# Kernel optimization log

Hardware: AMD Instinct MI355X
Metric: run time of the kernel (lower is better)

Reference implementation:

```python
import jax, jax.numpy as jnp
import numpy as np

N_NODES = 50000
N_EDGES = 400000
N_GRAPHS = 512
IN_DIM = 768
HID = 64
BN_EPS = 1e-5


def setup_inputs() -> dict:
    key = jax.random.key(0)
    ks = jax.random.split(key, 12)
    x = jax.random.normal(ks[0], (N_NODES, IN_DIM), dtype=jnp.float32)
    edge_index = jax.random.randint(ks[1], (2, N_EDGES), 0, N_NODES, dtype=jnp.int64)
    batch = jnp.sort(jax.random.randint(ks[2], (N_NODES,), 0, N_GRAPHS, dtype=jnp.int64))

    def lin_init(k, fan_in, fan_out):
        kw, kb = jax.random.split(k)
        bound = 1.0 / np.sqrt(fan_in)
        W = jax.random.uniform(kw, (fan_in, fan_out), minval=-bound, maxval=bound, dtype=jnp.float32)
        b = jax.random.uniform(kb, (fan_out,), minval=-bound, maxval=bound, dtype=jnp.float32)
        return W, b

    w1a, b1a = lin_init(ks[3], IN_DIM, HID)
    w1b, b1b = lin_init(ks[4], HID, HID)
    w2a, b2a = lin_init(ks[5], HID, HID)
    w2b, b2b = lin_init(ks[6], HID, HID)
    wl, bl = lin_init(ks[7], 2 * HID, 2)

    ones = jnp.ones((HID,), jnp.float32)
    zeros = jnp.zeros((HID,), jnp.float32)
    return {
        "x": x, "edge_index": edge_index, "batch": batch,
        "w1a": w1a, "b1a": b1a, "g1": ones, "be1": zeros, "rm1": zeros, "rv1": ones,
        "w1b": w1b, "b1b": b1b,
        "w2a": w2a, "b2a": b2a, "g2": ones, "be2": zeros, "rm2": zeros, "rv2": ones,
        "w2b": w2b, "b2b": b2b,
        "wl": wl, "bl": bl,
    }


def _bn_eval(h, gamma, beta, rm, rv):
    # BatchNorm1d in eval mode: normalize with running stats
    return (h - rm) * (gamma * jax.lax.rsqrt(rv + BN_EPS)) + beta


def _gin_conv(x, src, dst, Wa, ba, gamma, beta, rm, rv, Wb, bb):
    # GINConv eps=0: h = MLP(x + sum_{j in N(i)} x_j); messages x[src] scatter-added to dst
    agg = jax.ops.segment_sum(x[src], dst, num_segments=N_NODES)
    h = x + agg
    h = jnp.dot(h, Wa) + ba
    h = jax.nn.relu(_bn_eval(h, gamma, beta, rm, rv))
    return jnp.dot(h, Wb) + bb


def reference(x, edge_index, batch,
              w1a, b1a, g1, be1, rm1, rv1, w1b, b1b,
              w2a, b2a, g2, be2, rm2, rv2, w2b, b2b,
              wl, bl):
    src, dst = edge_index[0], edge_index[1]
    # eval mode: dropout_edge and F.dropout are identity
    x1 = jax.nn.relu(_gin_conv(x, src, dst, w1a, b1a, g1, be1, rm1, rv1, w1b, b1b))
    x2 = jax.nn.relu(_gin_conv(x1, src, dst, w2a, b2a, g2, be2, rm2, rv2, w2b, b2b))
    x_jk = jnp.concatenate([x1, x2], axis=-1)  # [N, 2*HID]
    x_pool = jax.ops.segment_sum(x_jk, batch, num_segments=N_GRAPHS)  # [G, 2*HID]
    return jnp.dot(x_pool, wl) + bl  # [G, 2]
```

## Files before the change

### kernel.cpp

```cpp
#include <hip/hip_runtime.h>

constexpr int N_NODES  = 50000;
constexpr int N_EDGES  = 400000;
constexpr int N_GRAPHS = 512;
constexpr int IN_DIM   = 768;
constexpr int HID      = 64;
constexpr float BN_EPS = 1e-5f;
constexpr int CAP      = 64;

typedef __attribute__((ext_vector_type(8))) short bf16x8;
typedef __attribute__((ext_vector_type(4))) float f32x4;
typedef __attribute__((ext_vector_type(2))) float f32x2;

__device__ __forceinline__ unsigned int f2bf2(float lo, float hi) {
  unsigned int r;
  asm("v_cvt_pk_bf16_f32 %0, %1, %2" : "=v"(r) : "v"(lo), "v"(hi));
  return r;
}
__device__ __forceinline__ ushort f2bf1(float f) { return (ushort)f2bf2(f, f); }

__device__ __forceinline__ float bf2f(ushort u) {
  return __uint_as_float((unsigned int)u << 16);
}
__device__ __forceinline__ f32x2 unpk(unsigned int u) {
  f32x2 v;
  v.x = __uint_as_float(u << 16);
  v.y = __uint_as_float(u & 0xffff0000u);
  return v;
}

constexpr int W1A_E = HID * IN_DIM;
constexpr int WB_E  = HID * HID;
__global__ __launch_bounds__(256) void convert_all(
    const float* __restrict__ w1a, const float* __restrict__ w1b,
    const float* __restrict__ w2a, const float* __restrict__ w2b,
    const float* __restrict__ bl,
    ushort* __restrict__ WT, ushort* __restrict__ WT1b,
    ushort* __restrict__ WT2a, ushort* __restrict__ WT2b,
    float* __restrict__ out, int* __restrict__ cnt) {
  int i = blockIdx.x * 256 + threadIdx.x;
  if (i < W1A_E) {
    int c = i / IN_DIM, k = i - c * IN_DIM;
    WT[i] = f2bf1(w1a[(size_t)k * HID + c]);
    return;
  }
  int j = i - W1A_E;
  if (j < 3 * WB_E) {
    int w = j / WB_E, r = j - w * WB_E;
    int c = r / HID, k = r - c * HID;
    const float* W = (w == 0) ? w1b : (w == 1) ? w2a : w2b;
    ushort* D = (w == 0) ? WT1b : (w == 1) ? WT2a : WT2b;
    D[r] = f2bf1(W[(size_t)k * HID + c]);
    return;
  }
  int o = j - 3 * WB_E;
  if (o < N_GRAPHS * 2) { out[o] = bl[o & 1]; return; }
  int z = o - N_GRAPHS * 2;
  if (z < N_NODES) cnt[z] = 0;
}

constexpr int GB1 = (N_NODES + 127) / 128;
constexpr int BB  = (N_EDGES + 255) / 256;

__global__ __launch_bounds__(256) void gemm_build(const float* __restrict__ X,
                                                  const ushort* __restrict__ WT,
                                                  ushort* __restrict__ P,
                                                  const int* __restrict__ src,
                                                  const int* __restrict__ dst,
                                                  int* __restrict__ cnt,
                                                  int* __restrict__ bucket) {
  const int tid = threadIdx.x;

  if (blockIdx.x >= GB1) {
    int e = (blockIdx.x - GB1) * 256 + tid;
    if (e < N_EDGES) {
      int s = src[e];
      int d = dst[e];
      int slot = atomicAdd(&cnt[d], 1);
      if (slot < CAP) bucket[d * CAP + slot] = s << 6;
    }
    return;
  }

  __shared__ ushort xs[128][64];
  __shared__ ushort ws[64][64];
  const int row0 = blockIdx.x * 128;
  const int wave = tid >> 6, lane = tid & 63, quad = lane >> 4, l16 = lane & 15;

  const int srow = tid >> 1;
  const int sk   = (tid & 1) * 32;
  int gr = row0 + srow;
  gr = gr < N_NODES ? gr : N_NODES - 1;
  const float* xrow = &X[(size_t)gr * IN_DIM + sk];
  const int wrow = tid >> 2;
  const int wc0  = (tid & 3) * 2;
  const ushort* wrp = &WT[(size_t)wrow * IN_DIM + wc0 * 8];

  f32x4 acc[2][4] = {};

  float4 xv[8];
#pragma unroll
  for (int i = 0; i < 8; i++) xv[i] = *(const float4*)&xrow[i * 4];
  uint4 wv0 = *(const uint4*)&wrp[0];
  uint4 wv1 = *(const uint4*)&wrp[8];

  for (int kt = 0; kt < IN_DIM; kt += 64) {
    unsigned int xw[16];
#pragma unroll
    for (int i = 0; i < 8; i++) {
      xw[i * 2 + 0] = f2bf2(xv[i].x, xv[i].y);
      xw[i * 2 + 1] = f2bf2(xv[i].z, xv[i].w);
    }
#pragma unroll
    for (int j = 0; j < 4; j++)
      *(uint4*)&xs[srow][(((sk >> 3) + j) ^ (srow & 7)) * 8] = *(const uint4*)&xw[j * 4];
    *(uint4*)&ws[wrow][((wc0 + 0) ^ (wrow & 7)) * 8] = wv0;
    *(uint4*)&ws[wrow][((wc0 + 1) ^ (wrow & 7)) * 8] = wv1;

    if (kt + 64 < IN_DIM) {
#pragma unroll
      for (int i = 0; i < 8; i++) xv[i] = *(const float4*)&xrow[kt + 64 + i * 4];
      wv0 = *(const uint4*)&wrp[kt + 64];
      wv1 = *(const uint4*)&wrp[kt + 64 + 8];
    }
    __syncthreads();

    const int ar0 = wave * 32 + l16;
    const int ar1 = ar0 + 16;
#pragma unroll
    for (int ks = 0; ks < 2; ks++) {
      bf16x8 a0 = *(const bf16x8*)&xs[ar0][((ks * 4 + quad) ^ (ar0 & 7)) * 8];
      bf16x8 a1 = *(const bf16x8*)&xs[ar1][((ks * 4 + quad) ^ (ar1 & 7)) * 8];
#pragma unroll
      for (int ct = 0; ct < 4; ct++) {
        const int br = ct * 16 + l16;
        bf16x8 b = *(const bf16x8*)&ws[br][((ks * 4 + quad) ^ (br & 7)) * 8];
        acc[0][ct] = __builtin_amdgcn_mfma_f32_16x16x32_bf16(a0, b, acc[0][ct], 0, 0, 0);
        acc[1][ct] = __builtin_amdgcn_mfma_f32_16x16x32_bf16(a1, b, acc[1][ct], 0, 0, 0);
      }
    }
    __syncthreads();
  }

#pragma unroll
  for (int g2 = 0; g2 < 2; g2++)
#pragma unroll
    for (int ct = 0; ct < 4; ct++)
#pragma unroll
      for (int r = 0; r < 4; r++) {
        int row = row0 + wave * 32 + g2 * 16 + quad * 4 + r;
        if (row < N_NODES)
          P[(size_t)row * HID + ct * 16 + l16] = f2bf1(acc[g2][ct][r]);
      }
}

template <int CHAIN>
__global__ __launch_bounds__(256) void fused_mlp(
    const int* __restrict__ cnt, const int* __restrict__ bucket,
    const ushort* __restrict__ Pin,
    const float* __restrict__ bin, const float* __restrict__ g,
    const float* __restrict__ be, const float* __restrict__ rm,
    const float* __restrict__ rv,
    const ushort* __restrict__ WT1, const float* __restrict__ b1,
    const ushort* __restrict__ WT2, ushort* __restrict__ OUT2,
    const int* __restrict__ batch, const float* __restrict__ wlh,
    float* __restrict__ out) {
  __shared__ ushort xs[64][64];
  __shared__ ushort ws[64][64];
  __shared__ ushort ws2[CHAIN ? 64 : 1][64];
  __shared__ float sS[64], sT[64];
  __shared__ float gacc[N_GRAPHS * 2];
  __shared__ float wl_s[2 * HID];
  __shared__ int   sbatch[64];
  const int tid  = threadIdx.x;
  const int row0 = blockIdx.x * 64;
  const int srow = tid >> 2;
  const int sub  = tid & 3;
  const int qc0  = sub * 2;
  const int sub16 = sub * 16;

  int node = row0 + srow;
  node = node < N_NODES ? node : N_NODES - 1;
  const int c_raw = cnt[node];
  const int* bkt = &bucket[node * CAP];
  const int4 pre = *(const int4*)bkt;
  unsigned int sw[8];
  {
    const ushort* sp = &Pin[node * HID + sub16];
    *(uint4*)&sw[0] = *(const uint4*)&sp[0];
    *(uint4*)&sw[4] = *(const uint4*)&sp[8];
  }

  if (tid < 64) {
    int nb = row0 + tid;
    sbatch[tid] = batch[nb < N_NODES ? nb : N_NODES - 1];
    float s = g[tid] * rsqrtf(rv[tid] + BN_EPS);
    sS[tid] = s;
    sT[tid] = (bin[tid] - rm[tid]) * s + be[tid];
  }
  if (tid < 2 * HID) wl_s[tid] = wlh[tid];
  {
    uint4 w0 = *(const uint4*)&WT1[(size_t)srow * HID + qc0 * 8];
    uint4 w1 = *(const uint4*)&WT1[(size_t)srow * HID + qc0 * 8 + 8];
    *(uint4*)&ws[srow][((qc0 + 0) ^ (srow & 7)) * 8] = w0;
    *(uint4*)&ws[srow][((qc0 + 1) ^ (srow & 7)) * 8] = w1;
    if (CHAIN) {
      uint4 v0 = *(const uint4*)&WT2[(size_t)srow * HID + qc0 * 8];
      uint4 v1 = *(const uint4*)&WT2[(size_t)srow * HID + qc0 * 8 + 8];
      *(uint4*)&ws2[srow][((qc0 + 0) ^ (srow & 7)) * 8] = v0;
      *(uint4*)&ws2[srow][((qc0 + 1) ^ (srow & 7)) * 8] = v1;
    }
  }
  __syncthreads();

  {
    f32x2 acc2[8];
#pragma unroll
    for (int j = 0; j < 8; j++) acc2[j] = unpk(sw[j]);

    int c = c_raw < CAP ? c_raw : CAP;
    int i = 0;
    if (c >= 4) {
      int4 s4 = pre;
      for (; i + 4 <= c; i += 4) {
        const int4 cur = s4;
        if (i + 8 <= c) s4 = *(const int4*)&bkt[i + 4];
        unsigned int w0[8], w1[8], w2[8], w3[8];
        const ushort* p0 = &Pin[cur.x + sub16];
        const ushort* p1 = &Pin[cur.y + sub16];
        const ushort* p2 = &Pin[cur.z + sub16];
        const ushort* p3 = &Pin[cur.w + sub16];
        *(uint4*)&w0[0] = *(const uint4*)&p0[0]; *(uint4*)&w0[4] = *(const uint4*)&p0[8];
        *(uint4*)&w1[0] = *(const uint4*)&p1[0]; *(uint4*)&w1[4] = *(const uint4*)&p1[8];
        *(uint4*)&w2[0] = *(const uint4*)&p2[0]; *(uint4*)&w2[4] = *(const uint4*)&p2[8];
        *(uint4*)&w3[0] = *(const uint4*)&p3[0]; *(uint4*)&w3[4] = *(const uint4*)&p3[8];
#pragma unroll
        for (int j = 0; j < 8; j++)
          acc2[j] += (unpk(w0[j]) + unpk(w1[j])) + (unpk(w2[j]) + unpk(w3[j]));
      }
    }
    for (; i < c; i++) {
      const ushort* p0 = &Pin[bkt[i] + sub16];
      unsigned int w0[8];
      *(uint4*)&w0[0] = *(const uint4*)&p0[0]; *(uint4*)&w0[4] = *(const uint4*)&p0[8];
#pragma unroll
      for (int j = 0; j < 8; j++) acc2[j] += unpk(w0[j]);
    }

    unsigned int hw[8];
#pragma unroll
    for (int j = 0; j < 8; j++) {
      const int col = sub16 + j * 2;
      float x0 = fmaxf(fmaf(acc2[j].x, sS[col],     sT[col]),     0.0f);
      float x1 = fmaxf(fmaf(acc2[j].y, sS[col + 1], sT[col + 1]), 0.0f);
      hw[j] = f2bf2(x0, x1);
    }
    *(uint4*)&xs[srow][((qc0 + 0) ^ (srow & 7)) * 8] = *(const uint4*)&hw[0];
    *(uint4*)&xs[srow][((qc0 + 1) ^ (srow & 7)) * 8] = *(const uint4*)&hw[4];
  }
  const int g0 = sbatch[0], g1 = sbatch[63];
  for (int z = g0 * 2 + tid; z <= g1 * 2 + 1; z += 256) gacc[z] = 0.0f;
  __syncthreads();

  const int wave = tid >> 6, lane = tid & 63, quad = lane >> 4, l16 = lane & 15;
  const int ar = wave * 16 + l16, axor = ar & 7;

  f32x4 acc1[4] = {};
#pragma unroll
  for (int ks = 0; ks < 2; ks++) {
    bf16x8 a = *(const bf16x8*)&xs[ar][((ks * 4 + quad) ^ axor) * 8];
#pragma unroll
    for (int ct = 0; ct < 4; ct++) {
      const int br = ct * 16 + l16;
      bf16x8 b = *(const bf16x8*)&ws[br][((ks * 4 + quad) ^ (br & 7)) * 8];
      acc1[ct] = __builtin_amdgcn_mfma_f32_16x16x32_bf16(a, b, acc1[ct], 0, 0, 0);
    }
  }

  if (CHAIN) __syncthreads();

  float v[4][4];
#pragma unroll
  for (int ct = 0; ct < 4; ct++) {
    const float bo = b1[ct * 16 + l16];
#pragma unroll
    for (int r = 0; r < 4; r++) v[ct][r] = fmaxf(acc1[ct][r] + bo, 0.0f);
  }

  {
    float p0[4] = {}, p1[4] = {};
#pragma unroll
    for (int ct = 0; ct < 4; ct++) {
      const int col = ct * 16 + l16;
      const float w0 = wl_s[col * 2 + 0], w1 = wl_s[col * 2 + 1];
#pragma unroll
      for (int r = 0; r < 4; r++) {
        p0[r] = fmaf(v[ct][r], w0, p0[r]);
        p1[r] = fmaf(v[ct][r], w1, p1[r]);
      }
    }
#pragma unroll
    for (int m = 1; m < 16; m <<= 1) {
#pragma unroll
      for (int r = 0; r < 4; r++) {
        p0[r] += __shfl_xor(p0[r], m);
        p1[r] += __shfl_xor(p1[r], m);
      }
    }
    if (l16 == 0) {
#pragma unroll
      for (int r = 0; r < 4; r++) {
        int lrow = wave * 16 + quad * 4 + r;
        if (row0 + lrow < N_NODES) {
          int gi = sbatch[lrow];
          atomicAdd(&gacc[gi * 2 + 0], p0[r]);
          atomicAdd(&gacc[gi * 2 + 1], p1[r]);
        }
      }
    }
  }

  if (CHAIN) {
#pragma unroll
    for (int ct = 0; ct < 4; ct++) {
      const int col = ct * 16 + l16;
#pragma unroll
      for (int r = 0; r < 4; r++) {
        int lrow = wave * 16 + quad * 4 + r;
        xs[lrow][(((col >> 3) ^ (lrow & 7)) * 8) + (col & 7)] = f2bf1(v[ct][r]);
      }
    }
    __syncthreads();

    f32x4 accB[4] = {};
#pragma unroll
    for (int ks = 0; ks < 2; ks++) {
      bf16x8 a = *(const bf16x8*)&xs[ar][((ks * 4 + quad) ^ axor) * 8];
#pragma unroll
      for (int ct = 0; ct < 4; ct++) {
        const int br = ct * 16 + l16;
        bf16x8 b = *(const bf16x8*)&ws2[br][((ks * 4 + quad) ^ (br & 7)) * 8];
        accB[ct] = __builtin_amdgcn_mfma_f32_16x16x32_bf16(a, b, accB[ct], 0, 0, 0);
      }
    }
#pragma unroll
    for (int ct = 0; ct < 4; ct++) {
      const int col = ct * 16 + l16;
#pragma unroll
      for (int r = 0; r < 4; r++) {
        int grow = row0 + wave * 16 + quad * 4 + r;
        if (grow < N_NODES) OUT2[(size_t)grow * HID + col] = f2bf1(accB[ct][r]);
      }
    }
  }

  __syncthreads();
  for (int z = g0 * 2 + tid; z <= g1 * 2 + 1; z += 256) {
    float vv = gacc[z];
    if (vv != 0.0f) atomicAdd(&out[z], vv);
  }
}

extern "C" void kernel_launch(void* const* d_in, const int* in_sizes, int n_in,
                              void* d_out, int out_size, void* d_ws, size_t ws_size,
                              hipStream_t stream) {
  const float* x   = (const float*)d_in[0];
  const int*   ei  = (const int*)d_in[1];
  const int*   bat = (const int*)d_in[2];
  const float* w1a = (const float*)d_in[3];
  const float* b1a = (const float*)d_in[4];
  const float* g1  = (const float*)d_in[5];
  const float* be1 = (const float*)d_in[6];
  const float* rm1 = (const float*)d_in[7];
  const float* rv1 = (const float*)d_in[8];
  const float* w1b = (const float*)d_in[9];
  const float* b1b = (const float*)d_in[10];
  const float* w2a = (const float*)d_in[11];
  const float* b2a = (const float*)d_in[12];
  const float* g2  = (const float*)d_in[13];
  const float* be2 = (const float*)d_in[14];
  const float* rm2 = (const float*)d_in[15];
  const float* rv2 = (const float*)d_in[16];
  const float* w2b = (const float*)d_in[17];
  const float* b2b = (const float*)d_in[18];
  const float* wl  = (const float*)d_in[19];
  const float* bl  = (const float*)d_in[20];
  float* out = (float*)d_out;

  const int* src = ei;
  const int* dst = ei + N_EDGES;

  const size_t FB = (size_t)N_NODES * HID;
  ushort* P1   = (ushort*)d_ws;
  ushort* P2   = P1 + FB;
  ushort* WT   = P2 + FB;
  ushort* WT1b = WT + (size_t)W1A_E;
  ushort* WT2a = WT1b + WB_E;
  ushort* WT2b = WT2a + WB_E;
  int* cnt     = (int*)(WT2b + WB_E);
  int* bucket  = cnt + N_NODES;

  const int GBF = (N_NODES + 63) / 64;
  const int CB  = (W1A_E + 3 * WB_E + N_GRAPHS * 2 + N_NODES + 255) / 256;

  convert_all<<<CB, 256, 0, stream>>>(w1a, w1b, w2a, w2b, bl,
                                      WT, WT1b, WT2a, WT2b, out, cnt);
  gemm_build<<<GB1 + BB, 256, 0, stream>>>(x, WT, P1, src, dst, cnt, bucket);
  fused_mlp<1><<<GBF, 256, 0, stream>>>(cnt, bucket, P1, b1a, g1, be1, rm1, rv1,
                                        WT1b, b1b, WT2a, P2, bat, wl, out);
  fused_mlp<0><<<GBF, 256, 0, stream>>>(cnt, bucket, P2, b2a, g2, be2, rm2, rv2,
                                        WT2b, b2b, nullptr, nullptr, bat,
                                        wl + 2 * HID, out);
}
```

Before: 304.7 us.

## Fuse weight conversion into GEMM, double-buffer LDS, shrink pooling accumulator

Removes the separate weight-conversion kernel: w1a is read as fp32 and converted to bf16 inside the GEMM tile loader, small weight conversions and output init move into the edge-bucketing blocks, and the count array is cleared with a memset. The GEMM K-loop uses double-buffered LDS to drop one barrier per iteration. The pooling accumulator in the MLP kernel shrinks to a small per-block window, with a fallback to global atomics. This trades one launch for redundant per-block weight conversion and more LDS per GEMM block.

```diff
diff --git a/kernel.cpp b/kernel.cpp
--- a/kernel.cpp
+++ b/kernel.cpp
@@ -19,9 +19,6 @@
 }
 __device__ __forceinline__ ushort f2bf1(float f) { return (ushort)f2bf2(f, f); }
 
-__device__ __forceinline__ float bf2f(ushort u) {
-  return __uint_as_float((unsigned int)u << 16);
-}
 __device__ __forceinline__ f32x2 unpk(unsigned int u) {
   f32x2 v;
   v.x = __uint_as_float(u << 16);
@@ -29,61 +26,46 @@
   return v;
 }
 
-constexpr int W1A_E = HID * IN_DIM;
-constexpr int WB_E  = HID * HID;
-__global__ __launch_bounds__(256) void convert_all(
-    const float* __restrict__ w1a, const float* __restrict__ w1b,
-    const float* __restrict__ w2a, const float* __restrict__ w2b,
-    const float* __restrict__ bl,
-    ushort* __restrict__ WT, ushort* __restrict__ WT1b,
-    ushort* __restrict__ WT2a, ushort* __restrict__ WT2b,
-    float* __restrict__ out, int* __restrict__ cnt) {
-  int i = blockIdx.x * 256 + threadIdx.x;
-  if (i < W1A_E) {
-    int c = i / IN_DIM, k = i - c * IN_DIM;
-    WT[i] = f2bf1(w1a[(size_t)k * HID + c]);
-    return;
-  }
-  int j = i - W1A_E;
-  if (j < 3 * WB_E) {
-    int w = j / WB_E, r = j - w * WB_E;
-    int c = r / HID, k = r - c * HID;
-    const float* W = (w == 0) ? w1b : (w == 1) ? w2a : w2b;
-    ushort* D = (w == 0) ? WT1b : (w == 1) ? WT2a : WT2b;
-    D[r] = f2bf1(W[(size_t)k * HID + c]);
-    return;
-  }
-  int o = j - 3 * WB_E;
-  if (o < N_GRAPHS * 2) { out[o] = bl[o & 1]; return; }
-  int z = o - N_GRAPHS * 2;
-  if (z < N_NODES) cnt[z] = 0;
-}
-
-constexpr int GB1 = (N_NODES + 127) / 128;
-constexpr int BB  = (N_EDGES + 255) / 256;
-
-__global__ __launch_bounds__(256) void gemm_build(const float* __restrict__ X,
-                                                  const ushort* __restrict__ WT,
-                                                  ushort* __restrict__ P,
-                                                  const int* __restrict__ src,
-                                                  const int* __restrict__ dst,
-                                                  int* __restrict__ cnt,
-                                                  int* __restrict__ bucket) {
+constexpr int WB_E = HID * HID;
+constexpr int GB1  = (N_NODES + 127) / 128;
+constexpr int BB   = (N_EDGES + 255) / 256;
+constexpr int CVB  = (3 * WB_E) / 256;
+
+__global__ __launch_bounds__(256) void gemm_build(
+    const float* __restrict__ X, const float* __restrict__ w1a,
+    ushort* __restrict__ P,
+    const int* __restrict__ src, const int* __restrict__ dst,
+    int* __restrict__ cnt, int* __restrict__ bucket,
+    const float* __restrict__ w1b, const float* __restrict__ w2a,
+    const float* __restrict__ w2b, const float* __restrict__ bl,
+    ushort* __restrict__ WT1b, ushort* __restrict__ WT2a,
+    ushort* __restrict__ WT2b, float* __restrict__ out) {
   const int tid = threadIdx.x;
 
   if (blockIdx.x >= GB1) {
-    int e = (blockIdx.x - GB1) * 256 + tid;
+    const int b = blockIdx.x - GB1;
+    int e = b * 256 + tid;
     if (e < N_EDGES) {
       int s = src[e];
       int d = dst[e];
       int slot = atomicAdd(&cnt[d], 1);
       if (slot < CAP) bucket[d * CAP + slot] = s << 6;
     }
+    if (b < CVB) {
+      int j = b * 256 + tid;
+      int w = j >> 12, r = j & (WB_E - 1);
+      int c = r >> 6, k = r & 63;
+      const float* W = (w == 0) ? w1b : (w == 1) ? w2a : w2b;
+      ushort* D = (w == 0) ? WT1b : (w == 1) ? WT2a : WT2b;
+      D[r] = f2bf1(W[k * HID + c]);
+    } else if (b == CVB) {
+      for (int o = tid; o < N_GRAPHS * 2; o += 256) out[o] = bl[o & 1];
+    }
     return;
   }
 
-  __shared__ ushort xs[128][64];
-  __shared__ ushort ws[64][64];
+  __shared__ ushort xs[2][128][64];
+  __shared__ ushort ws[2][64][64];
   const int row0 = blockIdx.x * 128;
   const int wave = tid >> 6, lane = tid & 63, quad = lane >> 4, l16 = lane & 15;
 
@@ -92,19 +74,23 @@
   int gr = row0 + srow;
   gr = gr < N_NODES ? gr : N_NODES - 1;
   const float* xrow = &X[(size_t)gr * IN_DIM + sk];
-  const int wrow = tid >> 2;
-  const int wc0  = (tid & 3) * 2;
-  const ushort* wrp = &WT[(size_t)wrow * IN_DIM + wc0 * 8];
+  const int wc  = tid & 63;
+  const int wj0 = (tid >> 6) * 2;
 
   f32x4 acc[2][4] = {};
 
   float4 xv[8];
+  float  wf[2][8];
 #pragma unroll
   for (int i = 0; i < 8; i++) xv[i] = *(const float4*)&xrow[i * 4];
-  uint4 wv0 = *(const uint4*)&wrp[0];
-  uint4 wv1 = *(const uint4*)&wrp[8];
-
-  for (int kt = 0; kt < IN_DIM; kt += 64) {
+#pragma unroll
+  for (int jj = 0; jj < 2; jj++)
+#pragma unroll
+    for (int i = 0; i < 8; i++)
+      wf[jj][i] = w1a[((wj0 + jj) * 8 + i) * HID + wc];
+
+  int t = 0;
+  for (int kt = 0; kt < IN_DIM; kt += 64, t ^= 1) {
     unsigned int xw[16];
 #pragma unroll
     for (int i = 0; i < 8; i++) {
@@ -113,15 +99,24 @@
     }
 #pragma unroll
     for (int j = 0; j < 4; j++)
-      *(uint4*)&xs[srow][(((sk >> 3) + j) ^ (srow & 7)) * 8] = *(const uint4*)&xw[j * 4];
-    *(uint4*)&ws[wrow][((wc0 + 0) ^ (wrow & 7)) * 8] = wv0;
-    *(uint4*)&ws[wrow][((wc0 + 1) ^ (wrow & 7)) * 8] = wv1;
+      *(uint4*)&xs[t][srow][(((sk >> 3) + j) ^ (srow & 7)) * 8] =
+          *(const uint4*)&xw[j * 4];
+#pragma unroll
+    for (int jj = 0; jj < 2; jj++) {
+      unsigned int pk[4];
+#pragma unroll
+      for (int q = 0; q < 4; q++) pk[q] = f2bf2(wf[jj][q * 2], wf[jj][q * 2 + 1]);
+      *(uint4*)&ws[t][wc][((wj0 + jj) ^ (wc & 7)) * 8] = *(const uint4*)&pk[0];
+    }
 
     if (kt + 64 < IN_DIM) {
 #pragma unroll
       for (int i = 0; i < 8; i++) xv[i] = *(const float4*)&xrow[kt + 64 + i * 4];
-      wv0 = *(const uint4*)&wrp[kt + 64];
-      wv1 = *(const uint4*)&wrp[kt + 64 + 8];
+#pragma unroll
+      for (int jj = 0; jj < 2; jj++)
+#pragma unroll
+        for (int i = 0; i < 8; i++)
+          wf[jj][i] = w1a[(kt + 64 + (wj0 + jj) * 8 + i) * HID + wc];
     }
     __syncthreads();
 
@@ -129,17 +124,16 @@
     const int ar1 = ar0 + 16;
 #pragma unroll
     for (int ks = 0; ks < 2; ks++) {
-      bf16x8 a0 = *(const bf16x8*)&xs[ar0][((ks * 4 + quad) ^ (ar0 & 7)) * 8];
-      bf16x8 a1 = *(const bf16x8*)&xs[ar1][((ks * 4 + quad) ^ (ar1 & 7)) * 8];
+      bf16x8 a0 = *(const bf16x8*)&xs[t][ar0][((ks * 4 + quad) ^ (ar0 & 7)) * 8];
+      bf16x8 a1 = *(const bf16x8*)&xs[t][ar1][((ks * 4 + quad) ^ (ar1 & 7)) * 8];
 #pragma unroll
       for (int ct = 0; ct < 4; ct++) {
         const int br = ct * 16 + l16;
-        bf16x8 b = *(const bf16x8*)&ws[br][((ks * 4 + quad) ^ (br & 7)) * 8];
+        bf16x8 b = *(const bf16x8*)&ws[t][br][((ks * 4 + quad) ^ (br & 7)) * 8];
         acc[0][ct] = __builtin_amdgcn_mfma_f32_16x16x32_bf16(a0, b, acc[0][ct], 0, 0, 0);
         acc[1][ct] = __builtin_amdgcn_mfma_f32_16x16x32_bf16(a1, b, acc[1][ct], 0, 0, 0);
       }
     }
-    __syncthreads();
   }
 
 #pragma unroll
@@ -169,7 +163,7 @@
   __shared__ ushort ws[64][64];
   __shared__ ushort ws2[CHAIN ? 64 : 1][64];
   __shared__ float sS[64], sT[64];
-  __shared__ float gacc[N_GRAPHS * 2];
+  __shared__ float gacc[64];
   __shared__ float wl_s[2 * HID];
   __shared__ int   sbatch[64];
   const int tid  = threadIdx.x;
@@ -194,6 +188,7 @@
   if (tid < 64) {
     int nb = row0 + tid;
     sbatch[tid] = batch[nb < N_NODES ? nb : N_NODES - 1];
+    gacc[tid] = 0.0f;
     float s = g[tid] * rsqrtf(rv[tid] + BN_EPS);
     sS[tid] = s;
     sT[tid] = (bin[tid] - rm[tid]) * s + be[tid];
@@ -212,6 +207,9 @@
     }
   }
   __syncthreads();
+
+  const int g0 = sbatch[0], g1 = sbatch[63];
+  const bool small = (g1 - g0) < 32;
 
   {
     f32x2 acc2[8];
@@ -258,8 +256,6 @@
     *(uint4*)&xs[srow][((qc0 + 0) ^ (srow & 7)) * 8] = *(const uint4*)&hw[0];
     *(uint4*)&xs[srow][((qc0 + 1) ^ (srow & 7)) * 8] = *(const uint4*)&hw[4];
   }
-  const int g0 = sbatch[0], g1 = sbatch[63];
-  for (int z = g0 * 2 + tid; z <= g1 * 2 + 1; z += 256) gacc[z] = 0.0f;
   __syncthreads();
 
   const int wave = tid >> 6, lane = tid & 63, quad = lane >> 4, l16 = lane & 15;
@@ -313,8 +309,13 @@
         int lrow = wave * 16 + quad * 4 + r;
         if (row0 + lrow < N_NODES) {
           int gi = sbatch[lrow];
-          atomicAdd(&gacc[gi * 2 + 0], p0[r]);
-          atomicAdd(&gacc[gi * 2 + 1], p1[r]);
+          if (small) {
+            atomicAdd(&gacc[(gi - g0) * 2 + 0], p0[r]);
+            atomicAdd(&gacc[(gi - g0) * 2 + 1], p1[r]);
+          } else {
+            atomicAdd(&out[gi * 2 + 0], p0[r]);
+            atomicAdd(&out[gi * 2 + 1], p1[r]);
+          }
         }
       }
     }
@@ -355,9 +356,12 @@
   }
 
   __syncthreads();
-  for (int z = g0 * 2 + tid; z <= g1 * 2 + 1; z += 256) {
-    float vv = gacc[z];
-    if (vv != 0.0f) atomicAdd(&out[z], vv);
+  if (small) {
+    const int span2 = (g1 - g0 + 1) * 2;
+    for (int z = tid; z < span2; z += 256) {
+      float vv = gacc[z];
+      if (vv != 0.0f) atomicAdd(&out[g0 * 2 + z], vv);
+    }
   }
 }
 
@@ -393,19 +397,18 @@
   const size_t FB = (size_t)N_NODES * HID;
   ushort* P1   = (ushort*)d_ws;
   ushort* P2   = P1 + FB;
-  ushort* WT   = P2 + FB;
-  ushort* WT1b = WT + (size_t)W1A_E;
+  ushort* WT1b = P2 + FB;
   ushort* WT2a = WT1b + WB_E;
   ushort* WT2b = WT2a + WB_E;
   int* cnt     = (int*)(WT2b + WB_E);
   int* bucket  = cnt + N_NODES;
 
   const int GBF = (N_NODES + 63) / 64;
-  const int CB  = (W1A_E + 3 * WB_E + N_GRAPHS * 2 + N_NODES + 255) / 256;
-
-  convert_all<<<CB, 256, 0, stream>>>(w1a, w1b, w2a, w2b, bl,
-                                      WT, WT1b, WT2a, WT2b, out, cnt);
-  gemm_build<<<GB1 + BB, 256, 0, stream>>>(x, WT, P1, src, dst, cnt, bucket);
+
+  hipMemsetAsync(cnt, 0, (size_t)N_NODES * sizeof(int), stream);
+  gemm_build<<<GB1 + BB, 256, 0, stream>>>(x, w1a, P1, src, dst, cnt, bucket,
+                                           w1b, w2a, w2b, bl,
+                                           WT1b, WT2a, WT2b, out);
   fused_mlp<1><<<GBF, 256, 0, stream>>>(cnt, bucket, P1, b1a, g1, be1, rm1, rv1,
                                         WT1b, b1b, WT2a, P2, bat, wl, out);
   fused_mlp<0><<<GBF, 256, 0, stream>>>(cnt, bucket, P2, b2a, g2, be2, rm2, rv2,
```

Result: no change. 307.7 us (+1.0%).

## Widen fused MLP blocks to 512 threads and split waves between GEMM stages

Applied to the files above, without the earlier changes.

The fused MLP kernel now runs with 512 threads per 64-row tile, so each thread gathers 8 columns instead of 16, which halves per-thread gather work and raises memory-level parallelism. In the chained variant, waves 0-3 run the first MFMA GEMM and pooling while waves 4-7 run the second GEMM, with one barrier between them. The shared-memory per-graph accumulator is shrunk to a 64-entry window relative to the tile's first graph, and tiles spanning 32 or more graphs fall back to global atomics. The cost is more threads per block and one more barrier, and the extra waves sit idle during the MFMA phase in the non-chained variant.

```diff
diff --git a/kernel.cpp b/kernel.cpp
--- a/kernel.cpp
+++ b/kernel.cpp
@@ -19,9 +19,6 @@
 }
 __device__ __forceinline__ ushort f2bf1(float f) { return (ushort)f2bf2(f, f); }
 
-__device__ __forceinline__ float bf2f(ushort u) {
-  return __uint_as_float((unsigned int)u << 16);
-}
 __device__ __forceinline__ f32x2 unpk(unsigned int u) {
   f32x2 v;
   v.x = __uint_as_float(u << 16);
@@ -61,6 +58,7 @@
 
 constexpr int GB1 = (N_NODES + 127) / 128;
 constexpr int BB  = (N_EDGES + 255) / 256;
+constexpr int GBF = (N_NODES + 63) / 64;
 
 __global__ __launch_bounds__(256) void gemm_build(const float* __restrict__ X,
                                                   const ushort* __restrict__ WT,
@@ -155,7 +153,7 @@
 }
 
 template <int CHAIN>
-__global__ __launch_bounds__(256) void fused_mlp(
+__global__ __launch_bounds__(512) void fused_mlp(
     const int* __restrict__ cnt, const int* __restrict__ bucket,
     const ushort* __restrict__ Pin,
     const float* __restrict__ bin, const float* __restrict__ g,
@@ -169,54 +167,47 @@
   __shared__ ushort ws[64][64];
   __shared__ ushort ws2[CHAIN ? 64 : 1][64];
   __shared__ float sS[64], sT[64];
-  __shared__ float gacc[N_GRAPHS * 2];
+  __shared__ float gacc[64];
   __shared__ float wl_s[2 * HID];
   __shared__ int   sbatch[64];
   const int tid  = threadIdx.x;
   const int row0 = blockIdx.x * 64;
-  const int srow = tid >> 2;
-  const int sub  = tid & 3;
-  const int qc0  = sub * 2;
-  const int sub16 = sub * 16;
+  const int srow = tid >> 3;
+  const int sub8 = tid & 7;
+  const int col0 = sub8 * 8;
 
   int node = row0 + srow;
   node = node < N_NODES ? node : N_NODES - 1;
   const int c_raw = cnt[node];
   const int* bkt = &bucket[node * CAP];
   const int4 pre = *(const int4*)bkt;
-  unsigned int sw[8];
-  {
-    const ushort* sp = &Pin[node * HID + sub16];
-    *(uint4*)&sw[0] = *(const uint4*)&sp[0];
-    *(uint4*)&sw[4] = *(const uint4*)&sp[8];
-  }
+  const uint4 swv = *(const uint4*)&Pin[node * HID + col0];
 
   if (tid < 64) {
     int nb = row0 + tid;
     sbatch[tid] = batch[nb < N_NODES ? nb : N_NODES - 1];
+    gacc[tid] = 0.0f;
     float s = g[tid] * rsqrtf(rv[tid] + BN_EPS);
     sS[tid] = s;
     sT[tid] = (bin[tid] - rm[tid]) * s + be[tid];
   }
   if (tid < 2 * HID) wl_s[tid] = wlh[tid];
   {
-    uint4 w0 = *(const uint4*)&WT1[(size_t)srow * HID + qc0 * 8];
-    uint4 w1 = *(const uint4*)&WT1[(size_t)srow * HID + qc0 * 8 + 8];
-    *(uint4*)&ws[srow][((qc0 + 0) ^ (srow & 7)) * 8] = w0;
-    *(uint4*)&ws[srow][((qc0 + 1) ^ (srow & 7)) * 8] = w1;
+    uint4 w0 = *(const uint4*)&WT1[(size_t)srow * HID + col0];
+    *(uint4*)&ws[srow][(sub8 ^ (srow & 7)) * 8] = w0;
     if (CHAIN) {
-      uint4 v0 = *(const uint4*)&WT2[(size_t)srow * HID + qc0 * 8];
-      uint4 v1 = *(const uint4*)&WT2[(size_t)srow * HID + qc0 * 8 + 8];
-      *(uint4*)&ws2[srow][((qc0 + 0) ^ (srow & 7)) * 8] = v0;
-      *(uint4*)&ws2[srow][((qc0 + 1) ^ (srow & 7)) * 8] = v1;
+      uint4 v0 = *(const uint4*)&WT2[(size_t)srow * HID + col0];
+      *(uint4*)&ws2[srow][(sub8 ^ (srow & 7)) * 8] = v0;
     }
   }
   __syncthreads();
 
   {
-    f32x2 acc2[8];
-#pragma unroll
-    for (int j = 0; j < 8; j++) acc2[j] = unpk(sw[j]);
+    unsigned int sw[4];
+    *(uint4*)&sw[0] = swv;
+    f32x2 acc2[4];
+#pragma unroll
+    for (int j = 0; j < 4; j++) acc2[j] = unpk(sw[j]);
 
     int c = c_raw < CAP ? c_raw : CAP;
     int i = 0;
@@ -225,69 +216,101 @@
       for (; i + 4 <= c; i += 4) {
         const int4 cur = s4;
         if (i + 8 <= c) s4 = *(const int4*)&bkt[i + 4];
-        unsigned int w0[8], w1[8], w2[8], w3[8];
-        const ushort* p0 = &Pin[cur.x + sub16];
-        const ushort* p1 = &Pin[cur.y + sub16];
-        const ushort* p2 = &Pin[cur.z + sub16];
-        const ushort* p3 = &Pin[cur.w + sub16];
-        *(uint4*)&w0[0] = *(const uint4*)&p0[0]; *(uint4*)&w0[4] = *(const uint4*)&p0[8];
-        *(uint4*)&w1[0] = *(const uint4*)&p1[0]; *(uint4*)&w1[4] = *(const uint4*)&p1[8];
-        *(uint4*)&w2[0] = *(const uint4*)&p2[0]; *(uint4*)&w2[4] = *(const uint4*)&p2[8];
-        *(uint4*)&w3[0] = *(const uint4*)&p3[0]; *(uint4*)&w3[4] = *(const uint4*)&p3[8];
-#pragma unroll
-        for (int j = 0; j < 8; j++)
+        unsigned int w0[4], w1[4], w2[4], w3[4];
+        *(uint4*)&w0[0] = *(const uint4*)&Pin[cur.x + col0];
+        *(uint4*)&w1[0] = *(const uint4*)&Pin[cur.y + col0];
+        *(uint4*)&w2[0] = *(const uint4*)&Pin[cur.z + col0];
+        *(uint4*)&w3[0] = *(const uint4*)&Pin[cur.w + col0];
+#pragma unroll
+        for (int j = 0; j < 4; j++)
           acc2[j] += (unpk(w0[j]) + unpk(w1[j])) + (unpk(w2[j]) + unpk(w3[j]));
       }
     }
     for (; i < c; i++) {
-      const ushort* p0 = &Pin[bkt[i] + sub16];
-      unsigned int w0[8];
-      *(uint4*)&w0[0] = *(const uint4*)&p0[0]; *(uint4*)&w0[4] = *(const uint4*)&p0[8];
-#pragma unroll
-      for (int j = 0; j < 8; j++) acc2[j] += unpk(w0[j]);
-    }
-
-    unsigned int hw[8];
-#pragma unroll
-    for (int j = 0; j < 8; j++) {
-      const int col = sub16 + j * 2;
+      unsigned int w0[4];
+      *(uint4*)&w0[0] = *(const uint4*)&Pin[bkt[i] + col0];
+#pragma unroll
+      for (int j = 0; j < 4; j++) acc2[j] += unpk(w0[j]);
+    }
+
+    unsigned int hw[4];
+#pragma unroll
+    for (int j = 0; j < 4; j++) {
+      const int col = col0 + j * 2;
       float x0 = fmaxf(fmaf(acc2[j].x, sS[col],     sT[col]),     0.0f);
       float x1 = fmaxf(fmaf(acc2[j].y, sS[col + 1], sT[col + 1]), 0.0f);
       hw[j] = f2bf2(x0, x1);
     }
-    *(uint4*)&xs[srow][((qc0 + 0) ^ (srow & 7)) * 8] = *(const uint4*)&hw[0];
-    *(uint4*)&xs[srow][((qc0 + 1) ^ (srow & 7)) * 8] = *(const uint4*)&hw[4];
-  }
-  const int g0 = sbatch[0], g1 = sbatch[63];
-  for (int z = g0 * 2 + tid; z <= g1 * 2 + 1; z += 256) gacc[z] = 0.0f;
+    *(uint4*)&xs[srow][(sub8 ^ (srow & 7)) * 8] = *(const uint4*)&hw[0];
+  }
   __syncthreads();
 
   const int wave = tid >> 6, lane = tid & 63, quad = lane >> 4, l16 = lane & 15;
-  const int ar = wave * 16 + l16, axor = ar & 7;
-
-  f32x4 acc1[4] = {};
-#pragma unroll
-  for (int ks = 0; ks < 2; ks++) {
-    bf16x8 a = *(const bf16x8*)&xs[ar][((ks * 4 + quad) ^ axor) * 8];
+  const int g0 = sbatch[0], g1v = sbatch[63];
+  const bool small = (g1v - g0) < 32;
+
+  float v[4][4];
+  if (wave < 4) {
+    const int ar = wave * 16 + l16, axor = ar & 7;
+    f32x4 acc1[4] = {};
+#pragma unroll
+    for (int ks = 0; ks < 2; ks++) {
+      bf16x8 a = *(const bf16x8*)&xs[ar][((ks * 4 + quad) ^ axor) * 8];
+#pragma unroll
+      for (int ct = 0; ct < 4; ct++) {
+        const int br = ct * 16 + l16;
+        bf16x8 b = *(const bf16x8*)&ws[br][((ks * 4 + quad) ^ (br & 7)) * 8];
+        acc1[ct] = __builtin_amdgcn_mfma_f32_16x16x32_bf16(a, b, acc1[ct], 0, 0, 0);
+      }
+    }
 #pragma unroll
     for (int ct = 0; ct < 4; ct++) {
-      const int br = ct * 16 + l16;
-      bf16x8 b = *(const bf16x8*)&ws[br][((ks * 4 + quad) ^ (br & 7)) * 8];
-      acc1[ct] = __builtin_amdgcn_mfma_f32_16x16x32_bf16(a, b, acc1[ct], 0, 0, 0);
-    }
-  }
-
-  if (CHAIN) __syncthreads();
-
-  float v[4][4];
-#pragma unroll
-  for (int ct = 0; ct < 4; ct++) {
-    const float bo = b1[ct * 16 + l16];
-#pragma unroll
-    for (int r = 0; r < 4; r++) v[ct][r] = fmaxf(acc1[ct][r] + bo, 0.0f);
-  }
-
-  {
+      const float bo = b1[ct * 16 + l16];
+#pragma unroll
+      for (int r = 0; r < 4; r++) v[ct][r] = fmaxf(acc1[ct][r] + bo, 0.0f);
+    }
+    if (CHAIN) {
+#pragma unroll
+      for (int ct = 0; ct < 4; ct++) {
+        const int col = ct * 16 + l16;
+#pragma unroll
+        for (int r = 0; r < 4; r++) {
+          int lrow = wave * 16 + quad * 4 + r;
+          xs[lrow][(((col >> 3) ^ (lrow & 7)) * 8) + (col & 7)] = f2bf1(v[ct][r]);
+        }
+      }
+    }
+  }
+
+  if (CHAIN) {
+    __syncthreads();
+    if (wave >= 4) {
+      const int wv = wave - 4;
+      const int ar = wv * 16 + l16, axor = ar & 7;
+      f32x4 accB[4] = {};
+#pragma unroll
+      for (int ks = 0; ks < 2; ks++) {
+        bf16x8 a = *(const bf16x8*)&xs[ar][((ks * 4 + quad) ^ axor) * 8];
+#pragma unroll
+        for (int ct = 0; ct < 4; ct++) {
+          const int br = ct * 16 + l16;
+          bf16x8 b = *(const bf16x8*)&ws2[br][((ks * 4 + quad) ^ (br & 7)) * 8];
+          accB[ct] = __builtin_amdgcn_mfma_f32_16x16x32_bf16(a, b, accB[ct], 0, 0, 0);
+        }
+      }
+#pragma unroll
+      for (int ct = 0; ct < 4; ct++) {
+        const int col = ct * 16 + l16;
+#pragma unroll
+        for (int r = 0; r < 4; r++) {
+          int grow = row0 + wv * 16 + quad * 4 + r;
+          if (grow < N_NODES) OUT2[(size_t)grow * HID + col] = f2bf1(accB[ct][r]);
+        }
+      }
+    }
+  }
+
+  if (wave < 4) {
     float p0[4] = {}, p1[4] = {};
 #pragma unroll
     for (int ct = 0; ct < 4; ct++) {
@@ -313,51 +336,25 @@
         int lrow = wave * 16 + quad * 4 + r;
         if (row0 + lrow < N_NODES) {
           int gi = sbatch[lrow];
-          atomicAdd(&gacc[gi * 2 + 0], p0[r]);
-          atomicAdd(&gacc[gi * 2 + 1], p1[r]);
+          if (small) {
+            atomicAdd(&gacc[(gi - g0) * 2 + 0], p0[r]);
+            atomicAdd(&gacc[(gi - g0) * 2 + 1], p1[r]);
+          } else {
+            atomicAdd(&out[gi * 2 + 0], p0[r]);
+            atomicAdd(&out[gi * 2 + 1], p1[r]);
+          }
         }
       }
     }
   }
 
-  if (CHAIN) {
-#pragma unroll
-    for (int ct = 0; ct < 4; ct++) {
-      const int col = ct * 16 + l16;
-#pragma unroll
-      for (int r = 0; r < 4; r++) {
-        int lrow = wave * 16 + quad * 4 + r;
-        xs[lrow][(((col >> 3) ^ (lrow & 7)) * 8) + (col & 7)] = f2bf1(v[ct][r]);
-      }
-    }
-    __syncthreads();
-
-    f32x4 accB[4] = {};
-#pragma unroll
-    for (int ks = 0; ks < 2; ks++) {
-      bf16x8 a = *(const bf16x8*)&xs[ar][((ks * 4 + quad) ^ axor) * 8];
-#pragma unroll
-      for (int ct = 0; ct < 4; ct++) {
-        const int br = ct * 16 + l16;
-        bf16x8 b = *(const bf16x8*)&ws2[br][((ks * 4 + quad) ^ (br & 7)) * 8];
-        accB[ct] = __builtin_amdgcn_mfma_f32_16x16x32_bf16(a, b, accB[ct], 0, 0, 0);
-      }
-    }
-#pragma unroll
-    for (int ct = 0; ct < 4; ct++) {
-      const int col = ct * 16 + l16;
-#pragma unroll
-      for (int r = 0; r < 4; r++) {
-        int grow = row0 + wave * 16 + quad * 4 + r;
-        if (grow < N_NODES) OUT2[(size_t)grow * HID + col] = f2bf1(accB[ct][r]);
-      }
-    }
-  }
-
   __syncthreads();
-  for (int z = g0 * 2 + tid; z <= g1 * 2 + 1; z += 256) {
-    float vv = gacc[z];
-    if (vv != 0.0f) atomicAdd(&out[z], vv);
+  if (small) {
+    const int span2 = (g1v - g0 + 1) * 2;
+    for (int z = tid; z < span2; z += 512) {
+      float vv = gacc[z];
+      if (vv != 0.0f) atomicAdd(&out[g0 * 2 + z], vv);
+    }
   }
 }
 
@@ -400,15 +397,14 @@
   int* cnt     = (int*)(WT2b + WB_E);
   int* bucket  = cnt + N_NODES;
 
-  const int GBF = (N_NODES + 63) / 64;
-  const int CB  = (W1A_E + 3 * WB_E + N_GRAPHS * 2 + N_NODES + 255) / 256;
+  const int CB = (W1A_E + 3 * WB_E + N_GRAPHS * 2 + N_NODES + 255) / 256;
 
   convert_all<<<CB, 256, 0, stream>>>(w1a, w1b, w2a, w2b, bl,
                                       WT, WT1b, WT2a, WT2b, out, cnt);
   gemm_build<<<GB1 + BB, 256, 0, stream>>>(x, WT, P1, src, dst, cnt, bucket);
-  fused_mlp<1><<<GBF, 256, 0, stream>>>(cnt, bucket, P1, b1a, g1, be1, rm1, rv1,
+  fused_mlp<1><<<GBF, 512, 0, stream>>>(cnt, bucket, P1, b1a, g1, be1, rm1, rv1,
                                         WT1b, b1b, WT2a, P2, bat, wl, out);
-  fused_mlp<0><<<GBF, 256, 0, stream>>>(cnt, bucket, P2, b2a, g2, be2, rm2, rv2,
+  fused_mlp<0><<<GBF, 512, 0, stream>>>(cnt, bucket, P2, b2a, g2, be2, rm2, rv2,
                                         WT2b, b2b, nullptr, nullptr, bat,
                                         wl + 2 * HID, out);
 }
```

Result: no change. 304.1 us (-0.2%).
